# Kernel optimization log

Measured on AMD Instinct MI355X. Metric: run time of the kernel, lower is better.

Reference implementation:

```python
import jax, jax.numpy as jnp
import numpy as np

R, N, H, DEPTH = 8, 65536, 128, 3  # regions, points, hidden width, hidden layers
W0 = 30.0  # SIREN frequency


def _make_boxes():
    # 2x2x2 non-overlapping partition of the unit cube -> [R, 3, 2] (min, max per axis)
    e = np.array([0.0, 0.5, 1.0], np.float32)
    boxes = []
    for i in range(2):
        for j in range(2):
            for k in range(2):
                boxes.append([[e[i], e[i + 1]], [e[j], e[j + 1]], [e[k], e[k + 1]]])
    return jnp.asarray(np.array(boxes, np.float32))


def setup_inputs() -> dict:
    key = jax.random.key(0)
    ks = jax.random.split(key, 8)
    x = jax.random.uniform(ks[0], (N, 3), dtype=jnp.float32)  # points in unit cube
    sd = lambda k, shape, fan: jax.random.normal(k, shape, jnp.float32) / np.sqrt(np.float32(fan))
    return {
        "x": x,
        "W_in": sd(ks[1], (R, 3, H), 3),
        "b_in": 0.01 * jax.random.normal(ks[2], (R, H), jnp.float32),
        "W_h": sd(ks[3], (R, DEPTH, H, H), H),
        "b_h": 0.01 * jax.random.normal(ks[4], (R, DEPTH, H), jnp.float32),
        "W_out": sd(ks[5], (R, H, 1), H),
        "b_out": 0.01 * jax.random.normal(ks[6], (R, 1), jnp.float32),
        "input_scale": jnp.ones((R, 3), jnp.float32),
        "boxes": _make_boxes(),
    }


def reference(x, W_in, b_in, W_h, b_h, W_out, b_out, input_scale, boxes):
    # lo/hi: [R, 1, 3]
    lo = boxes[:, :, 0][:, None, :]
    hi = boxes[:, :, 1][:, None, :]
    # AABox.norm_coord: map box -> [-1, 1], then per-region input_scale. [R, N, 3]
    xn = (2.0 * (x[None] - lo) / (hi - lo) - 1.0) * input_scale[:, None, :]
    # per-region SIREN MLP, vectorized over regions (r) and points (n)
    h = jnp.sin(W0 * (jnp.einsum('rnd,rdh->rnh', xn, W_in) + b_in[:, None, :]))
    for l in range(DEPTH):
        h = jnp.sin(W0 * (jnp.einsum('rnh,rhk->rnk', h, W_h[:, l]) + b_h[:, l][:, None, :]))
    vis = (jnp.einsum('rnh,rho->rno', h, W_out) + b_out[:, None, :])[..., 0]  # [R, N]
    # AABox.contain routing: each point belongs to (at most) one region
    mask = jnp.all((x[None] >= lo) & (x[None] <= hi), axis=-1)  # [R, N]
    rid = jnp.argmax(mask, axis=0)  # first containing region
    valid = jnp.any(mask, axis=0)
    out = jnp.take_along_axis(vis, rid[None, :], axis=0)[0]  # [N]
    return jnp.where(valid, out, 0.0)  # points outside all boxes stay zero
```

## Files before the change

kernel.cpp:

```cpp
#include <hip/hip_runtime.h>
#include <math.h>

#define NREG  8
#define HDIM  128
#define NDEPTH 3
#define TP    64
#define STRIP 32
#define W0F   30.0f


__device__ __forceinline__ int region_of(float X, float Y, float Z, bool* valid) {
    *valid = (X >= 0.f) & (X <= 1.f) & (Y >= 0.f) & (Y <= 1.f) & (Z >= 0.f) & (Z <= 1.f);
    int i = (X > 0.5f) ? 1 : 0;
    int j = (Y > 0.5f) ? 1 : 0;
    int k = (Z > 0.5f) ? 1 : 0;
    return i * 4 + j * 2 + k;
}

__global__ __launch_bounds__(256) void k_count(const float* __restrict__ x, int n,
                                               int* __restrict__ ws) {
    __shared__ int h[NREG];
    if (threadIdx.x < NREG) h[threadIdx.x] = 0;
    __syncthreads();
    int i = blockIdx.x * 256 + threadIdx.x;
    if (i < n) {
        float X = x[3*i], Y = x[3*i+1], Z = x[3*i+2];
        bool valid;
        int r = region_of(X, Y, Z, &valid);
        if (valid) atomicAdd(&h[r], 1);
    }
    __syncthreads();
    if (threadIdx.x < NREG) atomicAdd(&ws[threadIdx.x], h[threadIdx.x]);
}

__global__ void k_prefix(int* __restrict__ ws) {
    if (threadIdx.x == 0) {
        int acc = 0;
        for (int r = 0; r < NREG; ++r) {
            ws[8 + r] = acc;
            ws[20 + r] = acc;
            acc += ws[r];
        }
        ws[8 + NREG] = acc;
    }
}

__global__ __launch_bounds__(256) void k_scatter(const float* __restrict__ x, int n,
                                                 int* __restrict__ ws,
                                                 int* __restrict__ idx,
                                                 float* __restrict__ out) {
    __shared__ int hist[NREG];
    __shared__ int base[NREG];
    const int tid = threadIdx.x;
    if (tid < NREG) hist[tid] = 0;
    __syncthreads();
    int i = blockIdx.x * 256 + tid;
    int r = 0, rank = 0;
    bool valid = false;
    if (i < n) {
        float X = x[3*i], Y = x[3*i+1], Z = x[3*i+2];
        r = region_of(X, Y, Z, &valid);
        if (valid) rank = atomicAdd(&hist[r], 1);
        else out[i] = 0.0f;
    }
    __syncthreads();
    if (tid < NREG) {
        int c = hist[tid];
        base[tid] = c ? atomicAdd(&ws[20 + tid], c) : 0;
    }
    __syncthreads();
    if (valid) idx[base[r] + rank] = i;
}


__global__ __launch_bounds__(256, 3) void k_mlp(
    const float* __restrict__ x,
    const float* __restrict__ W_in,  const float* __restrict__ b_in,
    const float* __restrict__ W_h,   const float* __restrict__ b_h,
    const float* __restrict__ W_out, const float* __restrict__ b_out,
    const float* __restrict__ scale, const float* __restrict__ boxes,
    const int* __restrict__ offsets, const int* __restrict__ idx,
    float* __restrict__ out)
{
    __shared__ __align__(16) float hA[HDIM][TP];
    __shared__ __align__(16) float Ws[STRIP * HDIM];
    __shared__ float bias[HDIM];
    __shared__ float xn_s[TP][3];
    __shared__ int   gidx[TP];

    const int tid = threadIdx.x;

    int r = -1, base = 0, cnt = 0;
    {
        int bid = blockIdx.x, acc = 0;
        for (int rr = 0; rr < NREG; ++rr) {
            int o0 = offsets[rr], o1 = offsets[rr + 1];
            int c = o1 - o0;
            int t = (c + TP - 1) / TP;
            if (bid < acc + t) {
                int tile = bid - acc;
                r = rr; base = o0 + tile * TP; cnt = c - tile * TP;
                break;
            }
            acc += t;
        }
    }
    if (r < 0) return;
    if (cnt > TP) cnt = TP;

    if (tid < TP) {
        int g = (tid < cnt) ? idx[base + tid] : -1;
        gidx[tid] = g;
        float xs[3] = {0.f, 0.f, 0.f};
        if (g >= 0) { xs[0] = x[3*g]; xs[1] = x[3*g+1]; xs[2] = x[3*g+2]; }
        #pragma unroll
        for (int d = 0; d < 3; ++d) {
            float lo = boxes[r*6 + d*2 + 0];
            float hi = boxes[r*6 + d*2 + 1];
            float xn = (2.0f * (xs[d] - lo) / (hi - lo) - 1.0f) * scale[r*3 + d];
            xn_s[tid][d] = (g >= 0) ? xn : 0.0f;
        }
    }
    for (int i = tid; i < 3 * HDIM; i += 256) Ws[i] = W_in[r * 3 * HDIM + i];
    for (int i = tid; i < HDIM; i += 256)     bias[i] = b_in[r * HDIM + i];
    __syncthreads();

    const int pg = tid & 15;
    const int kg = tid >> 4;
    const int p0 = pg * 4;
    const int k0 = kg * 8;

    {
        float xm[4][3];
        #pragma unroll
        for (int m = 0; m < 4; ++m) {
            xm[m][0] = xn_s[p0 + m][0];
            xm[m][1] = xn_s[p0 + m][1];
            xm[m][2] = xn_s[p0 + m][2];
        }
        #pragma unroll
        for (int kc = 0; kc < 8; ++kc) {
            int k = k0 + kc;
            float w0 = Ws[0 * HDIM + k];
            float w1 = Ws[1 * HDIM + k];
            float w2 = Ws[2 * HDIM + k];
            float bk = bias[k];
            float v[4];
            #pragma unroll
            for (int m = 0; m < 4; ++m) {
                float a = fmaf(xm[m][0], w0, fmaf(xm[m][1], w1, fmaf(xm[m][2], w2, bk)));
                v[m] = sinf(W0F * a);
            }
            *(float4*)&hA[k][p0] = make_float4(v[0], v[1], v[2], v[3]);
        }
    }

    for (int l = 0; l < NDEPTH; ++l) {
        const float* Wl = W_h + (size_t)(r * NDEPTH + l) * HDIM * HDIM;
        const float* bl = b_h + (r * NDEPTH + l) * HDIM;
        float accv[4][8];
        #pragma unroll
        for (int m = 0; m < 4; ++m)
            #pragma unroll
            for (int kc = 0; kc < 8; ++kc) accv[m][kc] = 0.f;

        for (int s = 0; s < HDIM / STRIP; ++s) {
            __syncthreads();
            #pragma unroll
            for (int i = 0; i < (STRIP * HDIM) / (256 * 4); ++i) {
                int off = (i * 256 + tid) * 4;
                *(float4*)&Ws[off] = *(const float4*)(Wl + (size_t)s * STRIP * HDIM + off);
            }
            if (s == 0)
                for (int i = tid; i < HDIM; i += 256) bias[i] = bl[i];
            __syncthreads();

            #pragma unroll 8
            for (int j = 0; j < STRIP; ++j) {
                int jj = s * STRIP + j;
                float4 a4 = *(const float4*)&hA[jj][p0];
                float4 wA = *(const float4*)&Ws[j * HDIM + k0];
                float4 wB = *(const float4*)&Ws[j * HDIM + k0 + 4];
                float av[4] = {a4.x, a4.y, a4.z, a4.w};
                float wv[8] = {wA.x, wA.y, wA.z, wA.w, wB.x, wB.y, wB.z, wB.w};
                #pragma unroll
                for (int m = 0; m < 4; ++m)
                    #pragma unroll
                    for (int kc = 0; kc < 8; ++kc)
                        accv[m][kc] = fmaf(av[m], wv[kc], accv[m][kc]);
            }
        }
        __syncthreads();
        #pragma unroll
        for (int kc = 0; kc < 8; ++kc) {
            int k = k0 + kc;
            float bk = bias[k];
            float v[4];
            #pragma unroll
            for (int m = 0; m < 4; ++m)
                v[m] = sinf(W0F * (accv[m][kc] + bk));
            *(float4*)&hA[k][p0] = make_float4(v[0], v[1], v[2], v[3]);
        }
    }
    __syncthreads();

    if (tid < HDIM) Ws[tid] = W_out[r * HDIM + tid];
    __syncthreads();
    if (tid < TP) {
        float sacc = 0.f;
        #pragma unroll 8
        for (int k = 0; k < HDIM; ++k)
            sacc = fmaf(hA[k][tid], Ws[k], sacc);
        sacc += b_out[r];
        int g = gidx[tid];
        if (g >= 0) out[g] = sacc;
    }
}


extern "C" void kernel_launch(void* const* d_in, const int* in_sizes, int n_in,
                              void* d_out, int out_size, void* d_ws, size_t ws_size,
                              hipStream_t stream) {
    const float* x      = (const float*)d_in[0];
    const float* W_in   = (const float*)d_in[1];
    const float* b_in   = (const float*)d_in[2];
    const float* W_h    = (const float*)d_in[3];
    const float* b_h    = (const float*)d_in[4];
    const float* W_out  = (const float*)d_in[5];
    const float* b_out  = (const float*)d_in[6];
    const float* scale  = (const float*)d_in[7];
    const float* boxes  = (const float*)d_in[8];
    float* out = (float*)d_out;

    int n = in_sizes[0] / 3;
    int* wsi = (int*)d_ws;
    int* idx = (int*)((char*)d_ws + 256);

    hipMemsetAsync(d_ws, 0, 256, stream);

    int nb = (n + 255) / 256;
    hipLaunchKernelGGL(k_count,   dim3(nb), dim3(256), 0, stream, x, n, wsi);
    hipLaunchKernelGGL(k_prefix,  dim3(1),  dim3(64),  0, stream, wsi);
    hipLaunchKernelGGL(k_scatter, dim3(nb), dim3(256), 0, stream, x, n, wsi, idx, out);

    int ntiles = (n + TP - 1) / TP + NREG;
    hipLaunchKernelGGL(k_mlp, dim3(ntiles), dim3(256), 0, stream,
                       x, W_in, b_in, W_h, b_h, W_out, b_out, scale, boxes,
                       wsi + 8, idx, out);
}
```

Before: 138.4 us.

## Read MLP weights as wave-uniform scalar loads instead of staging through LDS

The hidden-layer GEMM is restructured so each wave owns 32 output neurons and each lane owns one point. Weights are read straight from global memory at wave-uniform addresses (the readfirstlane k0 lets the compiler use scalar loads), which removes the LDS weight staging and the per-strip barriers. The output layer is reduced across waves through a small shared buffer. In exchange, each thread keeps 32 accumulators and the inner loop depends on scalar-cache throughput. Launch bounds are raised to 4 blocks per CU.

```diff
diff --git a/kernel.cpp b/kernel.cpp
--- a/kernel.cpp
+++ b/kernel.cpp
@@ -5,7 +5,6 @@
 #define HDIM  128
 #define NDEPTH 3
 #define TP    64
-#define STRIP 32
 #define W0F   30.0f
 
 
@@ -73,7 +72,7 @@
 }
 
 
-__global__ __launch_bounds__(256, 3) void k_mlp(
+__global__ __launch_bounds__(256, 4) void k_mlp(
     const float* __restrict__ x,
     const float* __restrict__ W_in,  const float* __restrict__ b_in,
     const float* __restrict__ W_h,   const float* __restrict__ b_h,
@@ -83,12 +82,12 @@
     float* __restrict__ out)
 {
     __shared__ __align__(16) float hA[HDIM][TP];
-    __shared__ __align__(16) float Ws[STRIP * HDIM];
-    __shared__ float bias[HDIM];
-    __shared__ float xn_s[TP][3];
-    __shared__ int   gidx[TP];
-
-    const int tid = threadIdx.x;
+    __shared__ float part[4][TP];
+
+    const int tid  = threadIdx.x;
+    const int wv   = tid >> 6;
+    const int lane = tid & 63;
+    const int k0   = __builtin_amdgcn_readfirstlane(wv << 5);
 
     int r = -1, base = 0, cnt = 0;
     {
@@ -108,112 +107,66 @@
     if (r < 0) return;
     if (cnt > TP) cnt = TP;
 
-    if (tid < TP) {
-        int g = (tid < cnt) ? idx[base + tid] : -1;
-        gidx[tid] = g;
-        float xs[3] = {0.f, 0.f, 0.f};
-        if (g >= 0) { xs[0] = x[3*g]; xs[1] = x[3*g+1]; xs[2] = x[3*g+2]; }
+    int g = (lane < cnt) ? idx[base + lane] : -1;
+    float xn0 = 0.f, xn1 = 0.f, xn2 = 0.f;
+    if (g >= 0) {
+        float lo0 = boxes[r*6 + 0], hi0 = boxes[r*6 + 1];
+        float lo1 = boxes[r*6 + 2], hi1 = boxes[r*6 + 3];
+        float lo2 = boxes[r*6 + 4], hi2 = boxes[r*6 + 5];
+        xn0 = (2.0f * (x[3*g+0] - lo0) / (hi0 - lo0) - 1.0f) * scale[r*3 + 0];
+        xn1 = (2.0f * (x[3*g+1] - lo1) / (hi1 - lo1) - 1.0f) * scale[r*3 + 1];
+        xn2 = (2.0f * (x[3*g+2] - lo2) / (hi2 - lo2) - 1.0f) * scale[r*3 + 2];
+    }
+
+    {
+        const float* Wr = W_in + r * 3 * HDIM + k0;
+        const float* br = b_in + r * HDIM + k0;
+        #pragma unroll 8
+        for (int c = 0; c < 32; ++c) {
+            float pre = fmaf(xn0, Wr[0*HDIM + c],
+                        fmaf(xn1, Wr[1*HDIM + c],
+                        fmaf(xn2, Wr[2*HDIM + c], br[c])));
+            hA[k0 + c][lane] = sinf(W0F * pre);
+        }
+    }
+    __syncthreads();
+
+    for (int l = 0; l < NDEPTH; ++l) {
+        const float* Wl = W_h + ((size_t)(r * NDEPTH + l)) * HDIM * HDIM + k0;
+        const float* bl = b_h + (r * NDEPTH + l) * HDIM + k0;
+        float acc[32];
         #pragma unroll
-        for (int d = 0; d < 3; ++d) {
-            float lo = boxes[r*6 + d*2 + 0];
-            float hi = boxes[r*6 + d*2 + 1];
-            float xn = (2.0f * (xs[d] - lo) / (hi - lo) - 1.0f) * scale[r*3 + d];
-            xn_s[tid][d] = (g >= 0) ? xn : 0.0f;
-        }
-    }
-    for (int i = tid; i < 3 * HDIM; i += 256) Ws[i] = W_in[r * 3 * HDIM + i];
-    for (int i = tid; i < HDIM; i += 256)     bias[i] = b_in[r * HDIM + i];
-    __syncthreads();
-
-    const int pg = tid & 15;
-    const int kg = tid >> 4;
-    const int p0 = pg * 4;
-    const int k0 = kg * 8;
-
-    {
-        float xm[4][3];
+        for (int c = 0; c < 32; ++c) acc[c] = bl[c];
+
+        #pragma unroll 2
+        for (int j = 0; j < HDIM; ++j) {
+            float a = hA[j][lane];
+            const float* wrow = Wl + (size_t)j * HDIM;
+            #pragma unroll
+            for (int c = 0; c < 32; ++c)
+                acc[c] = fmaf(a, wrow[c], acc[c]);
+        }
         #pragma unroll
-        for (int m = 0; m < 4; ++m) {
-            xm[m][0] = xn_s[p0 + m][0];
-            xm[m][1] = xn_s[p0 + m][1];
-            xm[m][2] = xn_s[p0 + m][2];
-        }
-        #pragma unroll
-        for (int kc = 0; kc < 8; ++kc) {
-            int k = k0 + kc;
-            float w0 = Ws[0 * HDIM + k];
-            float w1 = Ws[1 * HDIM + k];
-            float w2 = Ws[2 * HDIM + k];
-            float bk = bias[k];
-            float v[4];
-            #pragma unroll
-            for (int m = 0; m < 4; ++m) {
-                float a = fmaf(xm[m][0], w0, fmaf(xm[m][1], w1, fmaf(xm[m][2], w2, bk)));
-                v[m] = sinf(W0F * a);
-            }
-            *(float4*)&hA[k][p0] = make_float4(v[0], v[1], v[2], v[3]);
-        }
-    }
-
-    for (int l = 0; l < NDEPTH; ++l) {
-        const float* Wl = W_h + (size_t)(r * NDEPTH + l) * HDIM * HDIM;
-        const float* bl = b_h + (r * NDEPTH + l) * HDIM;
-        float accv[4][8];
-        #pragma unroll
-        for (int m = 0; m < 4; ++m)
-            #pragma unroll
-            for (int kc = 0; kc < 8; ++kc) accv[m][kc] = 0.f;
-
-        for (int s = 0; s < HDIM / STRIP; ++s) {
-            __syncthreads();
-            #pragma unroll
-            for (int i = 0; i < (STRIP * HDIM) / (256 * 4); ++i) {
-                int off = (i * 256 + tid) * 4;
-                *(float4*)&Ws[off] = *(const float4*)(Wl + (size_t)s * STRIP * HDIM + off);
-            }
-            if (s == 0)
-                for (int i = tid; i < HDIM; i += 256) bias[i] = bl[i];
-            __syncthreads();
-
-            #pragma unroll 8
-            for (int j = 0; j < STRIP; ++j) {
-                int jj = s * STRIP + j;
-                float4 a4 = *(const float4*)&hA[jj][p0];
-                float4 wA = *(const float4*)&Ws[j * HDIM + k0];
-                float4 wB = *(const float4*)&Ws[j * HDIM + k0 + 4];
-                float av[4] = {a4.x, a4.y, a4.z, a4.w};
-                float wv[8] = {wA.x, wA.y, wA.z, wA.w, wB.x, wB.y, wB.z, wB.w};
-                #pragma unroll
-                for (int m = 0; m < 4; ++m)
-                    #pragma unroll
-                    for (int kc = 0; kc < 8; ++kc)
-                        accv[m][kc] = fmaf(av[m], wv[kc], accv[m][kc]);
-            }
-        }
+        for (int c = 0; c < 32; ++c) acc[c] = sinf(W0F * acc[c]);
         __syncthreads();
         #pragma unroll
-        for (int kc = 0; kc < 8; ++kc) {
-            int k = k0 + kc;
-            float bk = bias[k];
-            float v[4];
-            #pragma unroll
-            for (int m = 0; m < 4; ++m)
-                v[m] = sinf(W0F * (accv[m][kc] + bk));
-            *(float4*)&hA[k][p0] = make_float4(v[0], v[1], v[2], v[3]);
-        }
-    }
-    __syncthreads();
-
-    if (tid < HDIM) Ws[tid] = W_out[r * HDIM + tid];
-    __syncthreads();
-    if (tid < TP) {
-        float sacc = 0.f;
+        for (int c = 0; c < 32; ++c) hA[k0 + c][lane] = acc[c];
+        __syncthreads();
+    }
+
+    {
+        const float* Wo = W_out + r * HDIM + k0;
+        float s = 0.f;
         #pragma unroll 8
-        for (int k = 0; k < HDIM; ++k)
-            sacc = fmaf(hA[k][tid], Ws[k], sacc);
-        sacc += b_out[r];
-        int g = gidx[tid];
-        if (g >= 0) out[g] = sacc;
+        for (int c = 0; c < 32; ++c)
+            s = fmaf(hA[k0 + c][lane], Wo[c], s);
+        part[wv][lane] = s;
+    }
+    __syncthreads();
+    if (wv == 0) {
+        float s = part[0][lane] + part[1][lane] + part[2][lane] + part[3][lane]
+                + b_out[r];
+        if (g >= 0) out[g] = s;
     }
 }
 
```

After: 178.0 us. +28.6%, slower.

## Read hidden-layer weights directly from global memory instead of staging in LDS

Applied to the files above, without the earlier changes.

Removes the shared-memory weight strip staging and its per-strip barriers in the hidden layers. Each thread now loads its 8 output-column weights straight from global memory (relying on L1/L2 caching), and biases and input weights are also read directly. The output projection is split across all four waves with a small partial-sum reduction, and the occupancy hint in launch bounds is dropped. This frees about 16KB of LDS and cuts synchronization, but every wave now issues redundant global loads for the same weight rows, which adds cache traffic and latency.

```diff
diff --git a/kernel.cpp b/kernel.cpp
--- a/kernel.cpp
+++ b/kernel.cpp
@@ -5,7 +5,6 @@
 #define HDIM  128
 #define NDEPTH 3
 #define TP    64
-#define STRIP 32
 #define W0F   30.0f
 
 
@@ -73,7 +72,7 @@
 }
 
 
-__global__ __launch_bounds__(256, 3) void k_mlp(
+__global__ __launch_bounds__(256) void k_mlp(
     const float* __restrict__ x,
     const float* __restrict__ W_in,  const float* __restrict__ b_in,
     const float* __restrict__ W_h,   const float* __restrict__ b_h,
@@ -83,8 +82,7 @@
     float* __restrict__ out)
 {
     __shared__ __align__(16) float hA[HDIM][TP];
-    __shared__ __align__(16) float Ws[STRIP * HDIM];
-    __shared__ float bias[HDIM];
+    __shared__ float part[4][TP];
     __shared__ float xn_s[TP][3];
     __shared__ int   gidx[TP];
 
@@ -121,16 +119,16 @@
             xn_s[tid][d] = (g >= 0) ? xn : 0.0f;
         }
     }
-    for (int i = tid; i < 3 * HDIM; i += 256) Ws[i] = W_in[r * 3 * HDIM + i];
-    for (int i = tid; i < HDIM; i += 256)     bias[i] = b_in[r * HDIM + i];
-    __syncthreads();
-
-    const int pg = tid & 15;
-    const int kg = tid >> 4;
-    const int p0 = pg * 4;
-    const int k0 = kg * 8;
+    __syncthreads();
+
+    const int pg  = tid & 15;
+    const int kg  = tid >> 4;
+    const int p0  = pg * 4;
+    const int k0c = kg * 8;
 
     {
+        const float* Wr = W_in + r * 3 * HDIM;
+        const float* br = b_in + r * HDIM;
         float xm[4][3];
         #pragma unroll
         for (int m = 0; m < 4; ++m) {
@@ -140,11 +138,11 @@
         }
         #pragma unroll
         for (int kc = 0; kc < 8; ++kc) {
-            int k = k0 + kc;
-            float w0 = Ws[0 * HDIM + k];
-            float w1 = Ws[1 * HDIM + k];
-            float w2 = Ws[2 * HDIM + k];
-            float bk = bias[k];
+            int k = k0c + kc;
+            float w0 = Wr[0 * HDIM + k];
+            float w1 = Wr[1 * HDIM + k];
+            float w2 = Wr[2 * HDIM + k];
+            float bk = br[k];
             float v[4];
             #pragma unroll
             for (int m = 0; m < 4; ++m) {
@@ -154,66 +152,66 @@
             *(float4*)&hA[k][p0] = make_float4(v[0], v[1], v[2], v[3]);
         }
     }
+    __syncthreads();
 
     for (int l = 0; l < NDEPTH; ++l) {
-        const float* Wl = W_h + (size_t)(r * NDEPTH + l) * HDIM * HDIM;
-        const float* bl = b_h + (r * NDEPTH + l) * HDIM;
-        float accv[4][8];
+        const float* Wl = W_h + ((size_t)(r * NDEPTH + l)) * HDIM * HDIM + k0c;
+        const float* bl = b_h + (r * NDEPTH + l) * HDIM + k0c;
+        float acc[4][8];
         #pragma unroll
         for (int m = 0; m < 4; ++m)
             #pragma unroll
-            for (int kc = 0; kc < 8; ++kc) accv[m][kc] = 0.f;
-
-        for (int s = 0; s < HDIM / STRIP; ++s) {
-            __syncthreads();
-            #pragma unroll
-            for (int i = 0; i < (STRIP * HDIM) / (256 * 4); ++i) {
-                int off = (i * 256 + tid) * 4;
-                *(float4*)&Ws[off] = *(const float4*)(Wl + (size_t)s * STRIP * HDIM + off);
-            }
-            if (s == 0)
-                for (int i = tid; i < HDIM; i += 256) bias[i] = bl[i];
-            __syncthreads();
-
-            #pragma unroll 8
-            for (int j = 0; j < STRIP; ++j) {
-                int jj = s * STRIP + j;
-                float4 a4 = *(const float4*)&hA[jj][p0];
-                float4 wA = *(const float4*)&Ws[j * HDIM + k0];
-                float4 wB = *(const float4*)&Ws[j * HDIM + k0 + 4];
-                float av[4] = {a4.x, a4.y, a4.z, a4.w};
-                float wv[8] = {wA.x, wA.y, wA.z, wA.w, wB.x, wB.y, wB.z, wB.w};
+            for (int kc = 0; kc < 8; ++kc) acc[m][kc] = 0.f;
+
+        #pragma unroll 4
+        for (int j = 0; j < HDIM; ++j) {
+            const float* wrow = Wl + (size_t)j * HDIM;
+            float4 wA = *(const float4*)(wrow);
+            float4 wB = *(const float4*)(wrow + 4);
+            float4 a4 = *(const float4*)&hA[j][p0];
+            float av[4] = {a4.x, a4.y, a4.z, a4.w};
+            float wv[8] = {wA.x, wA.y, wA.z, wA.w, wB.x, wB.y, wB.z, wB.w};
+            #pragma unroll
+            for (int m = 0; m < 4; ++m)
                 #pragma unroll
-                for (int m = 0; m < 4; ++m)
-                    #pragma unroll
-                    for (int kc = 0; kc < 8; ++kc)
-                        accv[m][kc] = fmaf(av[m], wv[kc], accv[m][kc]);
-            }
-        }
+                for (int kc = 0; kc < 8; ++kc)
+                    acc[m][kc] = fmaf(av[m], wv[kc], acc[m][kc]);
+        }
+
+        float4 bA = *(const float4*)(bl);
+        float4 bB = *(const float4*)(bl + 4);
+        float bb[8] = {bA.x, bA.y, bA.z, bA.w, bB.x, bB.y, bB.z, bB.w};
+        float v[4][8];
+        #pragma unroll
+        for (int m = 0; m < 4; ++m)
+            #pragma unroll
+            for (int kc = 0; kc < 8; ++kc)
+                v[m][kc] = sinf(W0F * (acc[m][kc] + bb[kc]));
+
         __syncthreads();
         #pragma unroll
-        for (int kc = 0; kc < 8; ++kc) {
-            int k = k0 + kc;
-            float bk = bias[k];
-            float v[4];
-            #pragma unroll
-            for (int m = 0; m < 4; ++m)
-                v[m] = sinf(W0F * (accv[m][kc] + bk));
-            *(float4*)&hA[k][p0] = make_float4(v[0], v[1], v[2], v[3]);
-        }
-    }
-    __syncthreads();
-
-    if (tid < HDIM) Ws[tid] = W_out[r * HDIM + tid];
-    __syncthreads();
-    if (tid < TP) {
-        float sacc = 0.f;
+        for (int kc = 0; kc < 8; ++kc)
+            *(float4*)&hA[k0c + kc][p0] = make_float4(v[0][kc], v[1][kc], v[2][kc], v[3][kc]);
+        __syncthreads();
+    }
+
+    {
+        const int wv_  = tid >> 6;
+        const int lane = tid & 63;
+        const int k0w  = wv_ * 32;
+        const float* Wo = W_out + r * HDIM + k0w;
+        float s = 0.f;
         #pragma unroll 8
-        for (int k = 0; k < HDIM; ++k)
-            sacc = fmaf(hA[k][tid], Ws[k], sacc);
-        sacc += b_out[r];
-        int g = gidx[tid];
-        if (g >= 0) out[g] = sacc;
+        for (int c = 0; c < 32; ++c)
+            s = fmaf(hA[k0w + c][lane], Wo[c], s);
+        part[wv_][lane] = s;
+        __syncthreads();
+        if (wv_ == 0) {
+            float o = part[0][lane] + part[1][lane] + part[2][lane] + part[3][lane]
+                    + b_out[r];
+            int g = gidx[lane];
+            if (g >= 0) out[g] = o;
+        }
     }
 }
 
```

New measurement: 155.6 us. 12.4% more time.
